# Kernel tuning notes

Hardware: AMD Instinct MI355X
Metric: run time of the kernel (lower is better)

The kernel has to match this reference:

```python
import jax, jax.numpy as jnp
import numpy as np

POOL = 7
IMAGE_SHAPE = (1024, 1024, 3)


def _crop_and_resize(fmap, boxes, pool):
    """TF-style crop_and_resize with extrapolation_value=0.
    fmap: [C, H, W]; boxes: [N, (y1,x1,y2,x2)] normalized. Returns [N, C, pool, pool]."""
    C, H, W = fmap.shape
    dt = fmap.dtype
    y1, x1, y2, x2 = boxes[:, 0], boxes[:, 1], boxes[:, 2], boxes[:, 3]
    g = jnp.arange(pool, dtype=dt) / (pool - 1)  # [P] in [0,1]
    ys = (y1[:, None] + g[None, :] * (y2 - y1)[:, None]) * (H - 1)  # [N,P]
    xs = (x1[:, None] + g[None, :] * (x2 - x1)[:, None]) * (W - 1)  # [N,P]
    y0f = jnp.floor(ys); x0f = jnp.floor(xs)
    ly = (ys - y0f).astype(dt); lx = (xs - x0f).astype(dt)
    y0 = jnp.clip(y0f.astype(jnp.int32), 0, H - 1)
    y1i = jnp.clip(y0 + 1, 0, H - 1)
    x0 = jnp.clip(x0f.astype(jnp.int32), 0, W - 1)
    x1i = jnp.clip(x0 + 1, 0, W - 1)
    vy = ((ys >= 0) & (ys <= H - 1)).astype(dt)  # extrapolation_value = 0 outside
    vx = ((xs >= 0) & (xs <= W - 1)).astype(dt)

    def at(yi, xi):
        # gather -> [C, N, P, P]
        return fmap[:, yi[:, :, None], xi[:, None, :]]

    wy0 = (1 - ly)[None, :, :, None]; wy1 = ly[None, :, :, None]
    wx0 = (1 - lx)[None, :, None, :]; wx1 = lx[None, :, None, :]
    val = (at(y0, x0) * wy0 + at(y1i, x0) * wy1) * wx0 \
        + (at(y0, x1i) * wy0 + at(y1i, x1i) * wy1) * wx1
    val = val * (vy[None, :, :, None] * vx[None, :, None, :])
    return jnp.transpose(val, (1, 0, 2, 3))  # [N, C, P, P]


def reference(boxes, p2, p3, p4, p5):
    """pyramid_roi_align: route each box to FPN level 2..5 via the 224-scale
    log2 heuristic, then CropAndResize(pool, pool, 0) from that level.
    Output order matches input box order (original sorts back by box_to_level)."""
    h = boxes[:, 2] - boxes[:, 0]
    w = boxes[:, 3] - boxes[:, 1]
    image_area = float(IMAGE_SHAPE[0] * IMAGE_SHAPE[1])
    roi_level = 4.0 + jnp.log2(jnp.sqrt(h * w) / (224.0 / np.sqrt(image_area)))
    roi_level = jnp.clip(jnp.round(roi_level).astype(jnp.int32), 2, 5)
    boxes_d = jax.lax.stop_gradient(boxes)  # level_boxes.detach() in original
    fmaps = [p2, p3, p4, p5]
    pooled = jnp.zeros((boxes.shape[0], p2.shape[0], POOL, POOL), dtype=p2.dtype)
    for i, level in enumerate(range(2, 6)):
        mask = (roi_level == level).astype(p2.dtype)[:, None, None, None]
        pooled = pooled + mask * _crop_and_resize(fmaps[i], boxes_d, POOL)
    return pooled


def setup_inputs():
    key = jax.random.key(0)
    kb, ks, k2, k3, k4, k5 = jax.random.split(key, 6)
    N, C = 1000, 256
    size = jax.random.uniform(ks, (N, 2), minval=0.02, maxval=0.9)
    tl = jax.random.uniform(kb, (N, 2)) * (1.0 - size)  # top-left so box stays in [0,1]
    boxes = jnp.concatenate([tl[:, 0:1], tl[:, 1:2],
                             tl[:, 0:1] + size[:, 0:1], tl[:, 1:2] + size[:, 1:2]], axis=1)
    p2 = jax.random.normal(k2, (C, 256, 256), jnp.float32)
    p3 = jax.random.normal(k3, (C, 128, 128), jnp.float32)
    p4 = jax.random.normal(k4, (C, 64, 64), jnp.float32)
    p5 = jax.random.normal(k5, (C, 32, 32), jnp.float32)
    return {"boxes": boxes, "p2": p2, "p3": p3, "p4": p4, "p5": p5}
```

## Files before the change

### kernel.cpp

```cpp
#include <hip/hip_runtime.h>


#define POOL 7
#define NCH  256
#define ELEMS_PER_BOX (NCH * POOL * POOL)
#define QCH 64
#define QELEMS (QCH * POOL * POOL)
#define CG 8
#define NGROUPS (QCH / CG)
#define ROWS 14
#define MAXS4 9
#define BUFSLOTS (CG * ROWS * MAXS4)
#define GROUP_OUT (CG * 49)

typedef float f2 __attribute__((ext_vector_type(2)));
typedef __attribute__((address_space(1))) const void* gas_ptr;
typedef __attribute__((address_space(3))) void*       las_ptr;

__global__ __launch_bounds__(256, 4) void roi_align_kernel(
    const float* __restrict__ boxes,
    const float* __restrict__ p2, const float* __restrict__ p3,
    const float* __restrict__ p4, const float* __restrict__ p5,
    float* __restrict__ out, int N)
{
    const int bid     = blockIdx.x;
    const int n       = bid >> 2;
    const int quarter = bid & 3;

    __shared__ float s_stage[2][BUFSLOTS * 4];
    __shared__ float s_a[49], s_b[49], s_w0[49], s_w1[49];
    __shared__ int   s_dx[49];
    __shared__ int   s_off0[49], s_off1[49];
    __shared__ int   s_rowoff[ROWS];
    __shared__ int   s_HW, s_xb0, s_s4, s_fast;
    __shared__ const float* s_fmap;

    const int tid = threadIdx.x;

    if (tid < 49) {
        const float by1 = boxes[4 * n + 0];
        const float bx1 = boxes[4 * n + 1];
        const float by2 = boxes[4 * n + 2];
        const float bx2 = boxes[4 * n + 3];
        const float h = by2 - by1;
        const float w = bx2 - bx1;
        float rl = 4.0f + log2f(sqrtf(h * w) / 0.21875f);
        int level = (int)rintf(rl);
        level = min(5, max(2, level));
        const int H = 256 >> (level - 2);
        const int W = H;
        const int py = tid / 7;
        const int px = tid - 7 * py;

        const float ty = (float)py / 6.0f;
        const float ys = (by1 + ty * (by2 - by1)) * (float)(H - 1);
        const float yf = floorf(ys);
        const float ly = ys - yf;
        int y0 = (int)yf; y0 = min(H - 1, max(0, y0));
        const int y1 = min(H - 1, y0 + 1);
        const float vy = (ys >= 0.0f && ys <= (float)(H - 1)) ? 1.0f : 0.0f;

        const float tx = (float)px / 6.0f;
        const float xs = (bx1 + tx * (bx2 - bx1)) * (float)(W - 1);
        const float xf = floorf(xs);
        const float lx = xs - xf;
        int x0 = (int)xf; x0 = min(W - 1, max(0, x0));
        const float vx = (xs >= 0.0f && xs <= (float)(W - 1)) ? 1.0f : 0.0f;
        const int xb = min(x0, W - 2);
        const bool edge = (x0 != xb);
        const float a = edge ? 0.0f : vx * (1.0f - lx);
        const float b = edge ? vx : vx * lx;

        const float xsA = bx1 * (float)(W - 1);
        int xA = (int)floorf(xsA); xA = min(W - 1, max(0, xA));
        const int xbA = min(xA, W - 2);
        const float xsB = bx2 * (float)(W - 1);
        int xB = (int)floorf(xsB); xB = min(W - 1, max(0, xB));
        const int xbB = min(xB, W - 2);
        const int xb0  = xbA & ~3;
        const int need = xbB + 2 - xb0;
        const int sa4  = (need + 3) >> 2;

        s_off0[tid] = y0 * W + xb;
        s_off1[tid] = y1 * W + xb;
        s_a[tid] = a;
        s_b[tid] = b;
        s_w0[tid] = vy * (1.0f - ly);
        s_w1[tid] = vy * ly;
        s_dx[tid] = xb - xb0;
        if (px == 0) {
            s_rowoff[2 * py]     = y0 * W;
            s_rowoff[2 * py + 1] = y1 * W;
        }
        if (tid == 0) {
            s_HW   = H * W;
            s_fmap = (level == 2) ? p2 : (level == 3) ? p3 : (level == 4) ? p4 : p5;
            s_xb0  = xb0;
            s_s4   = sa4 | 1;
            s_fast = (need <= 32) ? 1 : 0;
        }
    }
    __syncthreads();

    const int HW = s_HW;
    const float* __restrict__ lvl = s_fmap;
    float* __restrict__ op = out + (size_t)n * ELEMS_PER_BOX + quarter * QELEMS;

    const int c1  = tid / 49,  p1  = tid - 49 * c1;
    const int o2  = 256 + tid;
    const int c2  = o2 / 49,   p2i = o2 - 49 * c2;
    const bool act2 = (tid < GROUP_OUT - 256);

    const float a1 = s_a[p1],  b1 = s_b[p1],  w01 = s_w0[p1],  w11 = s_w1[p1];
    const float a2 = s_a[p2i], b2 = s_b[p2i], w02 = s_w0[p2i], w12 = s_w1[p2i];

    if (s_fast) {
        const int s4 = s_s4;
        const int S  = 4 * s4;
        const int nslots = CG * ROWS * s4;
        const unsigned lim = (unsigned)(NCH * HW - 4);
        const unsigned cb  = (unsigned)(quarter * QCH) * (unsigned)HW;
        const int xb0 = s_xb0;

        unsigned g0 = 0, g1 = 0, g2v = 0, g3 = 0;
#define SLOTMETA(bvar, k)                                                     \
        { const int idx = (k)*256 + tid;                                      \
          if (idx < nslots) {                                                 \
              const int rid = idx / s4;                                       \
              const int q   = idx - rid * s4;                                 \
              const int cl  = rid / 14;                                       \
              const int r   = rid - 14 * cl;                                  \
              bvar = cb + (unsigned)(cl * HW + s_rowoff[r] + xb0 + 4 * q);    \
          } }
        SLOTMETA(g0, 0) SLOTMETA(g1, 1) SLOTMETA(g2v, 2) SLOTMETA(g3, 3)
#undef SLOTMETA

        const int t1 = (c1 * ROWS + 2 * (p1 / 7)) * S + s_dx[p1];
        const int t2 = (c2 * ROWS + 2 * (p2i / 7)) * S + s_dx[p2i];

#define GLD(bvar, k, gs, sb)                                                  \
        { const int idx = (k)*256 + tid;                                      \
          if (idx < nslots) {                                                 \
              const unsigned o = min(bvar + (gs), lim);                       \
              __builtin_amdgcn_global_load_lds((gas_ptr)(lvl + o),            \
                  (las_ptr)((sb) + idx * 4), 16, 0, 0);                       \
          } }
#define ISSUE(g, bi)                                                          \
        { const unsigned gs = (unsigned)((g) * CG * HW);                      \
          float* sb = s_stage[bi];                                            \
          GLD(g0, 0, gs, sb) GLD(g1, 1, gs, sb)                               \
          GLD(g2v, 2, gs, sb) GLD(g3, 3, gs, sb) }
#define COMPUTE(g, bi)                                                        \
        { const float* st = s_stage[bi];                                      \
          { const float t00 = st[t1],     t01 = st[t1 + 1];                   \
            const float t10 = st[t1 + S], t11 = st[t1 + S + 1];               \
            op[(g) * GROUP_OUT + tid] =                                       \
                (t00 * a1 + t01 * b1) * w01 + (t10 * a1 + t11 * b1) * w11; }  \
          if (act2) {                                                         \
            const float u00 = st[t2],     u01 = st[t2 + 1];                   \
            const float u10 = st[t2 + S], u11 = st[t2 + S + 1];               \
            op[(g) * GROUP_OUT + 256 + tid] =                                 \
                (u00 * a2 + u01 * b2) * w02 + (u10 * a2 + u11 * b2) * w12; } }

        ISSUE(0, 0);
#pragma unroll
        for (int g = 0; g < NGROUPS; ++g) {
            __syncthreads();
            if (g + 1 < NGROUPS) ISSUE(g + 1, (g + 1) & 1);
            COMPUTE(g, g & 1);
        }
#undef GLD
#undef ISSUE
#undef COMPUTE
    } else {
        const int off01 = s_off0[p1],  off11 = s_off1[p1];
        const int off02 = s_off0[p2i], off12 = s_off1[p2i];
        const float* __restrict__ fbase = lvl + (size_t)(quarter * QCH) * HW;
        for (int g = 0; g < NGROUPS; ++g) {
            const float* pl1 = fbase + (size_t)(g * CG + c1) * HW;
            const f2 q0 = *(const f2*)(pl1 + off01);
            const f2 q1 = *(const f2*)(pl1 + off11);
            const float r0 = q0.x * a1 + q0.y * b1;
            const float r1 = q1.x * a1 + q1.y * b1;
            op[g * GROUP_OUT + tid] = r0 * w01 + r1 * w11;
            if (act2) {
                const float* pl2 = fbase + (size_t)(g * CG + c2) * HW;
                const f2 u0 = *(const f2*)(pl2 + off02);
                const f2 u1 = *(const f2*)(pl2 + off12);
                const float s0 = u0.x * a2 + u0.y * b2;
                const float s1 = u1.x * a2 + u1.y * b2;
                op[g * GROUP_OUT + 256 + tid] = s0 * w02 + s1 * w12;
            }
        }
    }
}

extern "C" void kernel_launch(void* const* d_in, const int* in_sizes, int n_in,
                              void* d_out, int out_size, void* d_ws, size_t ws_size,
                              hipStream_t stream) {
    const float* boxes = (const float*)d_in[0];
    const float* p2    = (const float*)d_in[1];
    const float* p3    = (const float*)d_in[2];
    const float* p4    = (const float*)d_in[3];
    const float* p5    = (const float*)d_in[4];
    float* out = (float*)d_out;
    const int N = in_sizes[0] / 4;

    roi_align_kernel<<<N * 4, 256, 0, stream>>>(boxes, p2, p3, p4, p5, out, N);
}
```

Before: 149.3 us.

## Give each wave its own staging slice to remove block-wide barriers

The fast path is restructured so that each of the four waves owns 16 channels and a private LDS slice. Each wave loads 4 channels per step with global_load_lds, waits on its own vmcnt, then computes its outputs. This replaces the double-buffered block-wide __syncthreads pipeline, so no barriers are needed across waves. The cost is that load/compute overlap now exists only between waves rather than through prefetch within a wave, and the wave-level LDS visibility relies on vmcnt alone.

```diff
diff --git a/kernel.cpp b/kernel.cpp
--- a/kernel.cpp
+++ b/kernel.cpp
@@ -5,12 +5,13 @@
 #define NCH  256
 #define ELEMS_PER_BOX (NCH * POOL * POOL)
 #define QCH 64
-#define QELEMS (QCH * POOL * POOL)
+#define WCH 16
+#define SCH 4
+#define NSTEPS 4
+#define ROWS 14
+#define SLOTS 512
 #define CG 8
-#define NGROUPS (QCH / CG)
-#define ROWS 14
-#define MAXS4 9
-#define BUFSLOTS (CG * ROWS * MAXS4)
+#define NGROUPS 8
 #define GROUP_OUT (CG * 49)
 
 typedef float f2 __attribute__((ext_vector_type(2)));
@@ -27,12 +28,12 @@
     const int n       = bid >> 2;
     const int quarter = bid & 3;
 
-    __shared__ float s_stage[2][BUFSLOTS * 4];
+    __shared__ float s_stage[4][SLOTS * 4];
     __shared__ float s_a[49], s_b[49], s_w0[49], s_w1[49];
     __shared__ int   s_dx[49];
     __shared__ int   s_off0[49], s_off1[49];
     __shared__ int   s_rowoff[ROWS];
-    __shared__ int   s_HW, s_xb0, s_s4, s_fast;
+    __shared__ int   s_HW, s_xb0, s_s4s, s_fast;
     __shared__ const float* s_fmap;
 
     const int tid = threadIdx.x;
@@ -96,7 +97,7 @@
             s_HW   = H * W;
             s_fmap = (level == 2) ? p2 : (level == 3) ? p3 : (level == 4) ? p4 : p5;
             s_xb0  = xb0;
-            s_s4   = sa4 | 1;
+            s_s4s  = sa4 | 1;
             s_fast = (need <= 32) ? 1 : 0;
         }
     }
@@ -104,92 +105,111 @@
 
     const int HW = s_HW;
     const float* __restrict__ lvl = s_fmap;
-    float* __restrict__ op = out + (size_t)n * ELEMS_PER_BOX + quarter * QELEMS;
-
-    const int c1  = tid / 49,  p1  = tid - 49 * c1;
-    const int o2  = 256 + tid;
-    const int c2  = o2 / 49,   p2i = o2 - 49 * c2;
-    const bool act2 = (tid < GROUP_OUT - 256);
-
-    const float a1 = s_a[p1],  b1 = s_b[p1],  w01 = s_w0[p1],  w11 = s_w1[p1];
-    const float a2 = s_a[p2i], b2 = s_b[p2i], w02 = s_w0[p2i], w12 = s_w1[p2i];
+    const int lane = tid & 63;
+    const int wave = tid >> 6;
 
     if (s_fast) {
-        const int s4 = s_s4;
-        const int S  = 4 * s4;
-        const int nslots = CG * ROWS * s4;
+        const int s4s = s_s4s;
+        const int S   = 4 * s4s;
+        const int nslots = 56 * s4s;
         const unsigned lim = (unsigned)(NCH * HW - 4);
-        const unsigned cb  = (unsigned)(quarter * QCH) * (unsigned)HW;
-        const int xb0 = s_xb0;
-
-        unsigned g0 = 0, g1 = 0, g2v = 0, g3 = 0;
-#define SLOTMETA(bvar, k)                                                     \
-        { const int idx = (k)*256 + tid;                                      \
+        float* const slice = s_stage[wave];
+        const int chbase = quarter * QCH + wave * WCH;
+        const unsigned cb0 = (unsigned)chbase * (unsigned)HW;
+
+        unsigned inv0, inv1, inv2, inv3, inv4, inv5, inv6, inv7;
+#define SLOTMETA(k, bvar)                                                     \
+        { const int idx = (k) * 64 + lane;                                    \
           if (idx < nslots) {                                                 \
-              const int rid = idx / s4;                                       \
-              const int q   = idx - rid * s4;                                 \
-              const int cl  = rid / 14;                                       \
-              const int r   = rid - 14 * cl;                                  \
-              bvar = cb + (unsigned)(cl * HW + s_rowoff[r] + xb0 + 4 * q);    \
-          } }
-        SLOTMETA(g0, 0) SLOTMETA(g1, 1) SLOTMETA(g2v, 2) SLOTMETA(g3, 3)
+              const int rid = idx / s4s;               \
+              const int q   = idx - rid * s4s;         \
+              const int cl  = rid / 14;                \
+              const int r   = rid - 14 * cl;           \
+              bvar = (unsigned)(cl * HW + s_rowoff[r] + s_xb0 + 4 * q);       \
+          } else bvar = 0x40000000u; }
+        SLOTMETA(0, inv0) SLOTMETA(1, inv1) SLOTMETA(2, inv2) SLOTMETA(3, inv3)
+        SLOTMETA(4, inv4) SLOTMETA(5, inv5) SLOTMETA(6, inv6) SLOTMETA(7, inv7)
 #undef SLOTMETA
 
-        const int t1 = (c1 * ROWS + 2 * (p1 / 7)) * S + s_dx[p1];
-        const int t2 = (c2 * ROWS + 2 * (p2i / 7)) * S + s_dx[p2i];
-
-#define GLD(bvar, k, gs, sb)                                                  \
-        { const int idx = (k)*256 + tid;                                      \
-          if (idx < nslots) {                                                 \
-              const unsigned o = min(bvar + (gs), lim);                       \
-              __builtin_amdgcn_global_load_lds((gas_ptr)(lvl + o),            \
-                  (las_ptr)((sb) + idx * 4), 16, 0, 0);                       \
-          } }
-#define ISSUE(g, bi)                                                          \
-        { const unsigned gs = (unsigned)((g) * CG * HW);                      \
-          float* sb = s_stage[bi];                                            \
-          GLD(g0, 0, gs, sb) GLD(g1, 1, gs, sb)                               \
-          GLD(g2v, 2, gs, sb) GLD(g3, 3, gs, sb) }
-#define COMPUTE(g, bi)                                                        \
-        { const float* st = s_stage[bi];                                      \
-          { const float t00 = st[t1],     t01 = st[t1 + 1];                   \
-            const float t10 = st[t1 + S], t11 = st[t1 + S + 1];               \
-            op[(g) * GROUP_OUT + tid] =                                       \
-                (t00 * a1 + t01 * b1) * w01 + (t10 * a1 + t11 * b1) * w11; }  \
-          if (act2) {                                                         \
-            const float u00 = st[t2],     u01 = st[t2 + 1];                   \
-            const float u10 = st[t2 + S], u11 = st[t2 + S + 1];               \
-            op[(g) * GROUP_OUT + 256 + tid] =                                 \
-                (u00 * a2 + u01 * b2) * w02 + (u10 * a2 + u11 * b2) * w12; } }
-
-        ISSUE(0, 0);
-#pragma unroll
-        for (int g = 0; g < NGROUPS; ++g) {
-            __syncthreads();
-            if (g + 1 < NGROUPS) ISSUE(g + 1, (g + 1) & 1);
-            COMPUTE(g, g & 1);
-        }
+        bool  act0, act1, act2_, act3;
+        int   to0, to1, to2, to3;
+        float aa0, bb0, w00, w10, aa1, bb1, w01, w11;
+        float aa2, bb2, w02, w12, aa3, bb3, w03, w13;
+#define CELLMETA(j, act, to, aa, bb, w0v, w1v)                                \
+        { const int oidx = (j) * 64 + lane;                                   \
+          act = (oidx < SCH * 49);                                            \
+          const int oc = min(oidx, SCH * 49 - 1);                             \
+          const int cc = oc / 49;                                             \
+          const int pp = oc - 49 * cc;                                        \
+          to  = (cc * ROWS + 2 * (pp / 7)) * S + s_dx[pp];                    \
+          aa = s_a[pp]; bb = s_b[pp]; w0v = s_w0[pp]; w1v = s_w1[pp]; }
+        CELLMETA(0, act0, to0, aa0, bb0, w00, w10)
+        CELLMETA(1, act1, to1, aa1, bb1, w01, w11)
+        CELLMETA(2, act2_, to2, aa2, bb2, w02, w12)
+        CELLMETA(3, act3, to3, aa3, bb3, w03, w13)
+#undef CELLMETA
+
+        float* __restrict__ opw =
+            out + (size_t)n * ELEMS_PER_BOX + (size_t)chbase * 49;
+
+        for (int s = 0; s < NSTEPS; ++s) {
+            const unsigned stepoff = cb0 + (unsigned)(s * SCH * HW);
+#define GLD(k, bvar)                                                          \
+            if ((k) * 64 < nslots) {                                          \
+                const unsigned o = min(stepoff + bvar, lim);                  \
+                __builtin_amdgcn_global_load_lds((gas_ptr)(lvl + o),          \
+                    (las_ptr)(slice + ((k) * 64 + lane) * 4), 16, 0, 0);      \
+            }
+            GLD(0, inv0) GLD(1, inv1) GLD(2, inv2) GLD(3, inv3)
+            GLD(4, inv4) GLD(5, inv5) GLD(6, inv6) GLD(7, inv7)
 #undef GLD
-#undef ISSUE
-#undef COMPUTE
+            asm volatile("s_waitcnt vmcnt(0)" ::: "memory");
+            __builtin_amdgcn_sched_barrier(0);
+
+            float* __restrict__ o_s = opw + s * (SCH * 49);
+#define CELL(j, act, to, aa, bb, w0v, w1v)                                    \
+            if (act) {                                                        \
+                const float t00 = slice[(to)],     t01 = slice[(to) + 1];     \
+                const float t10 = slice[(to) + S], t11 = slice[(to) + S + 1]; \
+                o_s[(j) * 64 + lane] =                                        \
+                    (t00 * aa + t01 * bb) * w0v + (t10 * aa + t11 * bb) * w1v;\
+            }
+            CELL(0, act0, to0, aa0, bb0, w00, w10)
+            CELL(1, act1, to1, aa1, bb1, w01, w11)
+            CELL(2, act2_, to2, aa2, bb2, w02, w12)
+            CELL(3, act3, to3, aa3, bb3, w03, w13)
+#undef CELL
+            __builtin_amdgcn_sched_barrier(0);
+            asm volatile("" ::: "memory");
+        }
     } else {
+        const int c1  = tid / 49,  p1  = tid - 49 * c1;
+        const int o2  = 256 + tid;
+        const int c2  = o2 / 49,   p2i = o2 - 49 * c2;
+        const bool act2 = (tid < GROUP_OUT - 256);
+
+        const float a1 = s_a[p1],  b1 = s_b[p1],  w01f = s_w0[p1],  w11f = s_w1[p1];
+        const float a2 = s_a[p2i], b2 = s_b[p2i], w02f = s_w0[p2i], w12f = s_w1[p2i];
         const int off01 = s_off0[p1],  off11 = s_off1[p1];
         const int off02 = s_off0[p2i], off12 = s_off1[p2i];
+
         const float* __restrict__ fbase = lvl + (size_t)(quarter * QCH) * HW;
+        float* __restrict__ op =
+            out + (size_t)n * ELEMS_PER_BOX + quarter * (QCH * 49);
         for (int g = 0; g < NGROUPS; ++g) {
             const float* pl1 = fbase + (size_t)(g * CG + c1) * HW;
             const f2 q0 = *(const f2*)(pl1 + off01);
             const f2 q1 = *(const f2*)(pl1 + off11);
             const float r0 = q0.x * a1 + q0.y * b1;
             const float r1 = q1.x * a1 + q1.y * b1;
-            op[g * GROUP_OUT + tid] = r0 * w01 + r1 * w11;
+            op[g * GROUP_OUT + tid] = r0 * w01f + r1 * w11f;
             if (act2) {
                 const float* pl2 = fbase + (size_t)(g * CG + c2) * HW;
                 const f2 u0 = *(const f2*)(pl2 + off02);
                 const f2 u1 = *(const f2*)(pl2 + off12);
                 const float s0 = u0.x * a2 + u0.y * b2;
                 const float s1 = u1.x * a2 + u1.y * b2;
-                op[g * GROUP_OUT + 256 + tid] = s0 * w02 + s1 * w12;
+                op[g * GROUP_OUT + 256 + tid] = s0 * w02f + s1 * w12f;
             }
         }
     }
```

After: 147.6 us. Within noise of the previous version (-1.1%).
